# Kernel tuning notes

Measured on AMD Instinct MI355X. Metric: run time of the kernel, lower is better.

The kernel has to match this reference:

```python
import jax, jax.numpy as jnp
import numpy as np

N_NODES = 100000
N_EDGES = 1600000
IN_CH = 50


def setup_inputs() -> dict:
    key = jax.random.key(0)
    ks = jax.random.split(key, 6)
    x = jax.random.normal(ks[0], (N_NODES, IN_CH), dtype=jnp.float32)
    edge_index = jax.random.randint(ks[1], (2, N_EDGES), 0, N_NODES, dtype=jnp.int32)
    # Glorot-ish scaled weights
    W1 = jax.random.normal(ks[2], (2 * IN_CH, 64), dtype=jnp.float32) * (1.0 / np.sqrt(2 * IN_CH))
    b1 = jnp.zeros((64,), jnp.float32)
    W2 = jax.random.normal(ks[3], (2 * 64, 32), dtype=jnp.float32) * (1.0 / np.sqrt(2 * 64))
    b2 = jnp.zeros((32,), jnp.float32)
    W3 = jax.random.normal(ks[4], (32, 1), dtype=jnp.float32) * (1.0 / np.sqrt(32))
    b3 = jnp.zeros((1,), jnp.float32)
    return {"x": x, "edge_index": edge_index, "W1": W1, "b1": b1,
            "W2": W2, "b2": b2, "W3": W3, "b3": b3}


def _sage_conv(x, src, dst, W, b, n_nodes):
    # mean aggregation of neighbor (source) features onto target nodes
    msg = x[src]                                             # [E, d] gather
    agg = jax.ops.segment_sum(msg, dst, num_segments=n_nodes)  # [N, d]
    cnt = jax.ops.segment_sum(jnp.ones(src.shape[0], x.dtype), dst,
                              num_segments=n_nodes)            # [N]
    mean = agg / jnp.maximum(cnt, 1.0)[:, None]
    h = jnp.concatenate([x, mean], axis=-1)                  # concat=True
    return h @ W + b


def reference(x, edge_index, W1, b1, W2, b2, W3, b3):
    src, dst = edge_index[0], edge_index[1]
    n = x.shape[0]
    h = jax.nn.relu(_sage_conv(x, src, dst, W1, b1, n))
    h = jax.nn.relu(_sage_conv(h, src, dst, W2, b2, n))
    return h @ W3 + b3  # [N, 1]
```

## Files before the change

### kernel.cpp

```cpp
#include <hip/hip_runtime.h>
#include <hip/hip_bf16.h>

#define N_NODES 100000
#define N_EDGES 1600000
#define IN_CH 50
#define NPB 256
#define NB ((N_NODES + NPB - 1) / NPB)
#define CAPLOG 13
#define EPB 4096
#define NBLK_A ((N_EDGES + EPB - 1) / EPB)
#define PAD_BLOCKS ((N_NODES * 64) / 1024)

__global__ __launch_bounds__(1024) void bin_pad_kernel(
    const int* __restrict__ src, const int* __restrict__ dst,
    int* __restrict__ cursor_rel, unsigned* __restrict__ binned,
    const float* __restrict__ x, unsigned short* __restrict__ xb) {
    if (blockIdx.x >= NBLK_A) {
        int t = (blockIdx.x - NBLK_A) * 1024 + threadIdx.x;
        int n = t >> 6, c = t & 63;
        float v = (c < IN_CH) ? x[n * IN_CH + c] : 0.0f;
        __hip_bfloat16 hb = __float2bfloat16(v);
        xb[t] = *(unsigned short*)&hb;
        return;
    }
    __shared__ int bc[NB];
    __shared__ int boff[NB];
    int t = threadIdx.x;
    if (t < NB) bc[t] = 0;
    __syncthreads();
    int e0 = blockIdx.x * EPB;
    int e1 = min(e0 + EPB, N_EDGES);
    for (int i = e0 + t; i < e1; i += 1024)
        atomicAdd(&bc[dst[i] >> 8], 1);
    __syncthreads();
    if (t < NB) {
        int v = bc[t];
        int rel = v ? atomicAdd(&cursor_rel[t], v) : 0;
        boff[t] = (t << CAPLOG) + rel;
        bc[t] = 0;
    }
    __syncthreads();
    for (int i = e0 + t; i < e1; i += 1024) {
        int d = dst[i];
        int b = d >> 8;
        int k = atomicAdd(&bc[b], 1);
        binned[boff[b] + k] = ((unsigned)(d & 255) << 17) | (unsigned)src[i];
    }
}

__global__ __launch_bounds__(1024) void bucket_fine(
    const unsigned* __restrict__ binned, const int* __restrict__ cursor_rel,
    int* __restrict__ cnt, int* __restrict__ row_start, int* __restrict__ csr_src) {
    __shared__ int lcnt[NPB];
    __shared__ int lofs[NPB];
    __shared__ int sc[NPB];
    int t = threadIdx.x;
    int b = blockIdx.x;
    int nbase = b * NPB;
    int bbase = b << CAPLOG;
    int ecnt  = cursor_rel[b];
    if (t < NPB) lcnt[t] = 0;
    __syncthreads();
    for (int i = t; i < ecnt; i += 1024)
        atomicAdd(&lcnt[(binned[bbase + i] >> 17) & 255], 1);
    __syncthreads();
    int v = (t < NPB) ? lcnt[t] : 0;
    if (t < NPB) sc[t] = v;
    __syncthreads();
    for (int off = 1; off < NPB; off <<= 1) {
        int tmp = (t < NPB && t >= off) ? sc[t - off] : 0;
        __syncthreads();
        if (t < NPB) sc[t] += tmp;
        __syncthreads();
    }
    if (t < NPB) {
        int excl = sc[t] - v;
        lofs[t] = excl;
        int n = nbase + t;
        if (n < N_NODES) { cnt[n] = v; row_start[n] = bbase + excl; }
    }
    __syncthreads();
    for (int i = t; i < ecnt; i += 1024) {
        unsigned p = binned[bbase + i];
        int d = (int)((p >> 17) & 255);
        int k = atomicAdd(&lofs[d], 1);
        csr_src[bbase + k] = (int)(p & 0x1FFFFu);
    }
}

__device__ __forceinline__ void upadd8(float* a, uint4 v, float p) {
    a[0] = fmaf(p, __uint_as_float(v.x << 16), a[0]);
    a[1] = fmaf(p, __uint_as_float(v.x & 0xffff0000u), a[1]);
    a[2] = fmaf(p, __uint_as_float(v.y << 16), a[2]);
    a[3] = fmaf(p, __uint_as_float(v.y & 0xffff0000u), a[3]);
    a[4] = fmaf(p, __uint_as_float(v.z << 16), a[4]);
    a[5] = fmaf(p, __uint_as_float(v.z & 0xffff0000u), a[5]);
    a[6] = fmaf(p, __uint_as_float(v.w << 16), a[6]);
    a[7] = fmaf(p, __uint_as_float(v.w & 0xffff0000u), a[7]);
}

#define WAVE_LDS_FENCE() __asm__ volatile("s_waitcnt lgkmcnt(0)" ::: "memory")

__device__ __forceinline__ void gather2(
    const unsigned short* __restrict__ featb, const int* __restrict__ csr_src,
    const int* __restrict__ row_start, const int* __restrict__ cnt,
    int nb, int lane, float acc[2][8]) {
    int g  = lane >> 3;
    int cw = (lane & 7) * 8;
    int start[2], deg[2], sv[2];
    #pragma unroll
    for (int i = 0; i < 2; ++i) {
        start[i] = row_start[nb + i];
        deg[i]   = cnt[nb + i];
        #pragma unroll
        for (int c = 0; c < 8; ++c) acc[i][c] = 0.f;
    }
    int dmax = max(deg[0], deg[1]);
    #pragma unroll
    for (int i = 0; i < 2; ++i)
        sv[i] = (lane < deg[i]) ? csr_src[start[i] + lane] : 0;

    #pragma unroll
    for (int cb = 0; cb < 64; cb += 16) {
        if (cb >= dmax) break;
        int s00 = __shfl(sv[0], cb + g);
        int s01 = __shfl(sv[0], cb + 8 + g);
        int s10 = __shfl(sv[1], cb + g);
        int s11 = __shfl(sv[1], cb + 8 + g);
        uint4 v00 = *(const uint4*)(featb + s00 * 64 + cw);
        uint4 v01 = *(const uint4*)(featb + s01 * 64 + cw);
        uint4 v10 = *(const uint4*)(featb + s10 * 64 + cw);
        uint4 v11 = *(const uint4*)(featb + s11 * 64 + cw);
        int rem0 = deg[0] - cb;
        int rem1 = deg[1] - cb;
        upadd8(acc[0], v00, (g < rem0) ? 1.f : 0.f);
        upadd8(acc[0], v01, (g + 8 < rem0) ? 1.f : 0.f);
        upadd8(acc[1], v10, (g < rem1) ? 1.f : 0.f);
        upadd8(acc[1], v11, (g + 8 < rem1) ? 1.f : 0.f);
    }
    if (dmax > 64) {
        for (int i = 0; i < 2; ++i) {
            for (int c0 = 64; c0 < deg[i]; c0 += 64) {
                int rem = deg[i] - c0; if (rem > 64) rem = 64;
                int sx = (lane < rem) ? csr_src[start[i] + c0 + lane] : 0;
                for (int cb = 0; cb < rem; cb += 16) {
                    int s0 = __shfl(sx, cb + g);
                    int s1 = __shfl(sx, cb + 8 + g);
                    float p0 = (cb + g < rem) ? 1.f : 0.f;
                    float p1 = (cb + 8 + g < rem) ? 1.f : 0.f;
                    uint4 v0 = *(const uint4*)(featb + s0 * 64 + cw);
                    uint4 v1 = *(const uint4*)(featb + s1 * 64 + cw);
                    upadd8(acc[i], v0, p0);
                    upadd8(acc[i], v1, p1);
                }
            }
        }
    }
    #pragma unroll
    for (int i = 0; i < 2; ++i) {
        float inv = 1.0f / fmaxf((float)deg[i], 1.0f);
        #pragma unroll
        for (int c = 0; c < 8; ++c) {
            float t = acc[i][c];
            t += __shfl_xor(t, 8);
            t += __shfl_xor(t, 16);
            t += __shfl_xor(t, 32);
            acc[i][c] = t * inv;
        }
    }
}

__device__ __forceinline__ float bf16u(unsigned short u) {
    return __uint_as_float(((unsigned)u) << 16);
}

__global__ __launch_bounds__(256, 8) void layer1_fused(
    const unsigned short* __restrict__ xb,
    const int* __restrict__ csr_src, const int* __restrict__ row_start,
    const int* __restrict__ cnt, const float* __restrict__ W1,
    const float* __restrict__ b1, unsigned short* __restrict__ h1b) {
    int wv   = threadIdx.x >> 6;
    int lane = threadIdx.x & 63;
    int nb   = (blockIdx.x * 4 + wv) * 2;

    float acc[2][8];
    gather2(xb, csr_src, row_start, cnt, nb, lane, acc);

    __shared__ __align__(16) float selfF[4][2][64];
    __shared__ __align__(16) float meanF[4][2][64];
    #pragma unroll
    for (int i = 0; i < 2; ++i) {
        selfF[wv][i][lane] = bf16u(xb[((nb + i) << 6) + lane]);
        if (lane < 8) {
            *(float4*)&meanF[wv][i][lane * 8] =
                make_float4(acc[i][0], acc[i][1], acc[i][2], acc[i][3]);
            *(float4*)&meanF[wv][i][lane * 8 + 4] =
                make_float4(acc[i][4], acc[i][5], acc[i][6], acc[i][7]);
        }
    }
    WAVE_LDS_FENCE();

    float ao[2];
    float bb = b1[lane];
    #pragma unroll
    for (int i = 0; i < 2; ++i) ao[i] = bb;
    #pragma unroll
    for (int k = 0; k < IN_CH; ++k) {
        float w = W1[k * 64 + lane];
        #pragma unroll
        for (int i = 0; i < 2; ++i) ao[i] = fmaf(selfF[wv][i][k], w, ao[i]);
    }
    #pragma unroll
    for (int k = 0; k < IN_CH; ++k) {
        float w = W1[(IN_CH + k) * 64 + lane];
        #pragma unroll
        for (int i = 0; i < 2; ++i) ao[i] = fmaf(meanF[wv][i][k], w, ao[i]);
    }
    #pragma unroll
    for (int i = 0; i < 2; ++i) {
        float r = fmaxf(ao[i], 0.f);
        __hip_bfloat16 hb = __float2bfloat16(r);
        h1b[((nb + i) << 6) + lane] = *(unsigned short*)&hb;
    }
}

__global__ __launch_bounds__(256) void transform_w2(
    const unsigned short* __restrict__ h1b,
    const float* __restrict__ W2, const float* __restrict__ b2,
    unsigned short* __restrict__ y2b, float* __restrict__ yselff) {
    __shared__ __align__(16) float sW2[4096];
    int t = threadIdx.x;
    #pragma unroll
    for (int i = 0; i < 16; ++i)
        sW2[t + i * 256] = W2[t + i * 256];
    __syncthreads();

    int lane = t & 63;
    int wv   = t >> 6;
    int hh   = lane >> 5;
    int j    = lane & 31;
    int node = blockIdx.x * 8 + wv * 2 + hh;
    unsigned hp = *(const unsigned*)(h1b + node * 64 + j * 2);
    float ys = b2[j], ym = 0.f;
    #pragma unroll
    for (int kk = 0; kk < 32; ++kk) {
        unsigned hv = __shfl(hp, kk, 32);
        float h0 = __uint_as_float(hv << 16);
        float h1 = __uint_as_float(hv & 0xffff0000u);
        ys = fmaf(h0, sW2[(2 * kk) * 32 + j], ys);
        ym = fmaf(h0, sW2[(64 + 2 * kk) * 32 + j], ym);
        ys = fmaf(h1, sW2[(2 * kk + 1) * 32 + j], ys);
        ym = fmaf(h1, sW2[(64 + 2 * kk + 1) * 32 + j], ym);
    }
    yselff[node * 32 + j] = ys;
    __hip_bfloat16 hb = __float2bfloat16(ym);
    y2b[node * 32 + j] = *(unsigned short*)&hb;
}

__global__ __launch_bounds__(256, 8) void layer23_fused(
    const unsigned short* __restrict__ y2b,
    const int* __restrict__ csr_src, const int* __restrict__ row_start,
    const int* __restrict__ cnt, const float* __restrict__ yselff,
    const float* __restrict__ W3, const float* __restrict__ b3,
    float* __restrict__ out) {
    int wv   = threadIdx.x >> 6;
    int lane = threadIdx.x & 63;
    int nb   = (blockIdx.x * 4 + wv) * 2;
    int g  = lane >> 2;
    int cw = (lane & 3) * 8;

    int start[2], deg[2], sv[2];
    float acc[2][8];
    #pragma unroll
    for (int i = 0; i < 2; ++i) {
        start[i] = row_start[nb + i];
        deg[i]   = cnt[nb + i];
        #pragma unroll
        for (int c = 0; c < 8; ++c) acc[i][c] = 0.f;
    }
    int dmax = max(deg[0], deg[1]);
    #pragma unroll
    for (int i = 0; i < 2; ++i)
        sv[i] = (lane < deg[i]) ? csr_src[start[i] + lane] : 0;

    #pragma unroll
    for (int cb = 0; cb < 64; cb += 32) {
        if (cb >= dmax) break;
        int s00 = __shfl(sv[0], cb + g);
        int s01 = __shfl(sv[0], cb + 16 + g);
        int s10 = __shfl(sv[1], cb + g);
        int s11 = __shfl(sv[1], cb + 16 + g);
        uint4 v00 = *(const uint4*)(y2b + s00 * 32 + cw);
        uint4 v01 = *(const uint4*)(y2b + s01 * 32 + cw);
        uint4 v10 = *(const uint4*)(y2b + s10 * 32 + cw);
        uint4 v11 = *(const uint4*)(y2b + s11 * 32 + cw);
        int rem0 = deg[0] - cb;
        int rem1 = deg[1] - cb;
        upadd8(acc[0], v00, (g < rem0) ? 1.f : 0.f);
        upadd8(acc[0], v01, (g + 16 < rem0) ? 1.f : 0.f);
        upadd8(acc[1], v10, (g < rem1) ? 1.f : 0.f);
        upadd8(acc[1], v11, (g + 16 < rem1) ? 1.f : 0.f);
    }
    if (dmax > 64) {
        for (int i = 0; i < 2; ++i) {
            for (int c0 = 64; c0 < deg[i]; c0 += 64) {
                int rem = deg[i] - c0; if (rem > 64) rem = 64;
                int sx = (lane < rem) ? csr_src[start[i] + c0 + lane] : 0;
                for (int cb = 0; cb < rem; cb += 32) {
                    int s0 = __shfl(sx, cb + g);
                    int s1 = __shfl(sx, cb + 16 + g);
                    float p0 = (cb + g < rem) ? 1.f : 0.f;
                    float p1 = (cb + 16 + g < rem) ? 1.f : 0.f;
                    uint4 v0 = *(const uint4*)(y2b + s0 * 32 + cw);
                    uint4 v1 = *(const uint4*)(y2b + s1 * 32 + cw);
                    upadd8(acc[i], v0, p0);
                    upadd8(acc[i], v1, p1);
                }
            }
        }
    }

    __shared__ __align__(16) float aggF[4][2][32];
    #pragma unroll
    for (int i = 0; i < 2; ++i) {
        float inv = 1.0f / fmaxf((float)deg[i], 1.0f);
        #pragma unroll
        for (int c = 0; c < 8; ++c) {
            float t = acc[i][c];
            t += __shfl_xor(t, 4);
            t += __shfl_xor(t, 8);
            t += __shfl_xor(t, 16);
            t += __shfl_xor(t, 32);
            acc[i][c] = t * inv;
        }
    }
    if (lane < 4) {
        #pragma unroll
        for (int i = 0; i < 2; ++i) {
            *(float4*)&aggF[wv][i][lane * 8] =
                make_float4(acc[i][0], acc[i][1], acc[i][2], acc[i][3]);
            *(float4*)&aggF[wv][i][lane * 8 + 4] =
                make_float4(acc[i][4], acc[i][5], acc[i][6], acc[i][7]);
        }
    }
    WAVE_LDS_FENCE();

    int hh = lane >> 5;
    int j  = lane & 31;
    float pre = yselff[(nb + hh) * 32 + j] + aggF[wv][hh][j];
    float v0 = fmaxf(pre, 0.f) * W3[j];
    #pragma unroll
    for (int off = 1; off <= 16; off <<= 1)
        v0 += __shfl_xor(v0, off);
    if (j == 0)
        out[nb + hh] = v0 + b3[0];
}

extern "C" void kernel_launch(void* const* d_in, const int* in_sizes, int n_in,
                              void* d_out, int out_size, void* d_ws, size_t ws_size,
                              hipStream_t stream) {
    const float* x   = (const float*)d_in[0];
    const int*   ei  = (const int*)d_in[1];
    const int*   src = ei;
    const int*   dst = ei + N_EDGES;
    const float* W1  = (const float*)d_in[2];
    const float* b1  = (const float*)d_in[3];
    const float* W2  = (const float*)d_in[4];
    const float* b2  = (const float*)d_in[5];
    const float* W3  = (const float*)d_in[6];
    const float* b3  = (const float*)d_in[7];
    float* out = (float*)d_out;

    char* ws = (char*)d_ws;
    auto align = [](size_t v) { return (v + 255) & ~(size_t)255; };
    size_t o = 0;
    int* cursor_rel = (int*)(ws + o); o = align(o + 512 * 4);
    int* cnt       = (int*)(ws + o); o = align(o + (size_t)N_NODES * 4);
    int* row_start = (int*)(ws + o); o = align(o + (size_t)N_NODES * 4);
    unsigned* binned = (unsigned*)(ws + o); o = align(o + ((size_t)NB << CAPLOG) * 4);
    int* csr_src   = (int*)(ws + o); o = align(o + ((size_t)NB << CAPLOG) * 4);
    unsigned short* xb  = (unsigned short*)(ws + o); o = align(o + (size_t)N_NODES * 64 * 2);
    unsigned short* h1b = (unsigned short*)(ws + o); o = align(o + (size_t)N_NODES * 64 * 2);
    unsigned short* y2b = (unsigned short*)(ws + o); o = align(o + (size_t)N_NODES * 32 * 2);
    float* yselff = (float*)(ws + o); o = align(o + (size_t)N_NODES * 32 * 4);

    (void)hipMemsetAsync(cursor_rel, 0, 512 * sizeof(int), stream);

    bin_pad_kernel<<<NBLK_A + PAD_BLOCKS, 1024, 0, stream>>>(src, dst, cursor_rel,
                                                             binned, x, xb);
    bucket_fine<<<NB, 1024, 0, stream>>>(binned, cursor_rel, cnt, row_start, csr_src);

    layer1_fused<<<N_NODES / 8, 256, 0, stream>>>(xb, csr_src, row_start, cnt,
                                                  W1, b1, h1b);
    transform_w2<<<N_NODES / 8, 256, 0, stream>>>(h1b, W2, b2, y2b, yselff);
    layer23_fused<<<N_NODES / 8, 256, 0, stream>>>(y2b, csr_src, row_start, cnt,
                                                   yselff, W3, b3, out);
}
```

Before: 264.7 us.

## Replace bucketed CSR build with global-atomic count/scan/scatter; restructure W2 transform

```diff
diff --git a/kernel.cpp b/kernel.cpp
--- a/kernel.cpp
+++ b/kernel.cpp
@@ -4,16 +4,12 @@
 #define N_NODES 100000
 #define N_EDGES 1600000
 #define IN_CH 50
-#define NPB 256
-#define NB ((N_NODES + NPB - 1) / NPB)
-#define CAPLOG 13
 #define EPB 4096
 #define NBLK_A ((N_EDGES + EPB - 1) / EPB)
 #define PAD_BLOCKS ((N_NODES * 64) / 1024)
 
-__global__ __launch_bounds__(1024) void bin_pad_kernel(
-    const int* __restrict__ src, const int* __restrict__ dst,
-    int* __restrict__ cursor_rel, unsigned* __restrict__ binned,
+__global__ __launch_bounds__(1024) void count_pad(
+    const int* __restrict__ dst, int* __restrict__ cnt,
     const float* __restrict__ x, unsigned short* __restrict__ xb) {
     if (blockIdx.x >= NBLK_A) {
         int t = (blockIdx.x - NBLK_A) * 1024 + threadIdx.x;
@@ -23,68 +19,41 @@
         xb[t] = *(unsigned short*)&hb;
         return;
     }
-    __shared__ int bc[NB];
-    __shared__ int boff[NB];
-    int t = threadIdx.x;
-    if (t < NB) bc[t] = 0;
-    __syncthreads();
     int e0 = blockIdx.x * EPB;
     int e1 = min(e0 + EPB, N_EDGES);
-    for (int i = e0 + t; i < e1; i += 1024)
-        atomicAdd(&bc[dst[i] >> 8], 1);
-    __syncthreads();
-    if (t < NB) {
-        int v = bc[t];
-        int rel = v ? atomicAdd(&cursor_rel[t], v) : 0;
-        boff[t] = (t << CAPLOG) + rel;
-        bc[t] = 0;
-    }
-    __syncthreads();
-    for (int i = e0 + t; i < e1; i += 1024) {
+    for (int i = e0 + threadIdx.x; i < e1; i += 1024)
+        atomicAdd(&cnt[dst[i]], 1);
+}
+
+__global__ __launch_bounds__(256) void alloc_rows(
+    const int* __restrict__ cnt, int* __restrict__ row_start,
+    int* __restrict__ gcur) {
+    int n = blockIdx.x * 256 + threadIdx.x;
+    int lane = threadIdx.x & 63;
+    int v = (n < N_NODES) ? cnt[n] : 0;
+    int s = v;
+    #pragma unroll
+    for (int off = 1; off < 64; off <<= 1) {
+        int t = __shfl_up(s, off);
+        if (lane >= off) s += t;
+    }
+    int total = __shfl(s, 63);
+    int base = 0;
+    if (lane == 63) base = atomicAdd(gcur, total);
+    base = __shfl(base, 63);
+    if (n < N_NODES) row_start[n] = base + s - v;
+}
+
+__global__ __launch_bounds__(1024) void scatter_csr(
+    const int* __restrict__ src, const int* __restrict__ dst,
+    const int* __restrict__ row_start, int* __restrict__ cur,
+    int* __restrict__ csr_src) {
+    int e0 = blockIdx.x * EPB;
+    int e1 = min(e0 + EPB, N_EDGES);
+    for (int i = e0 + threadIdx.x; i < e1; i += 1024) {
         int d = dst[i];
-        int b = d >> 8;
-        int k = atomicAdd(&bc[b], 1);
-        binned[boff[b] + k] = ((unsigned)(d & 255) << 17) | (unsigned)src[i];
-    }
-}
-
-__global__ __launch_bounds__(1024) void bucket_fine(
-    const unsigned* __restrict__ binned, const int* __restrict__ cursor_rel,
-    int* __restrict__ cnt, int* __restrict__ row_start, int* __restrict__ csr_src) {
-    __shared__ int lcnt[NPB];
-    __shared__ int lofs[NPB];
-    __shared__ int sc[NPB];
-    int t = threadIdx.x;
-    int b = blockIdx.x;
-    int nbase = b * NPB;
-    int bbase = b << CAPLOG;
-    int ecnt  = cursor_rel[b];
-    if (t < NPB) lcnt[t] = 0;
-    __syncthreads();
-    for (int i = t; i < ecnt; i += 1024)
-        atomicAdd(&lcnt[(binned[bbase + i] >> 17) & 255], 1);
-    __syncthreads();
-    int v = (t < NPB) ? lcnt[t] : 0;
-    if (t < NPB) sc[t] = v;
-    __syncthreads();
-    for (int off = 1; off < NPB; off <<= 1) {
-        int tmp = (t < NPB && t >= off) ? sc[t - off] : 0;
-        __syncthreads();
-        if (t < NPB) sc[t] += tmp;
-        __syncthreads();
-    }
-    if (t < NPB) {
-        int excl = sc[t] - v;
-        lofs[t] = excl;
-        int n = nbase + t;
-        if (n < N_NODES) { cnt[n] = v; row_start[n] = bbase + excl; }
-    }
-    __syncthreads();
-    for (int i = t; i < ecnt; i += 1024) {
-        unsigned p = binned[bbase + i];
-        int d = (int)((p >> 17) & 255);
-        int k = atomicAdd(&lofs[d], 1);
-        csr_src[bbase + k] = (int)(p & 0x1FFFFu);
+        int k = atomicAdd(&cur[d], 1);
+        csr_src[row_start[d] + k] = src[i];
     }
 }
 
@@ -228,33 +197,47 @@
     const unsigned short* __restrict__ h1b,
     const float* __restrict__ W2, const float* __restrict__ b2,
     unsigned short* __restrict__ y2b, float* __restrict__ yselff) {
-    __shared__ __align__(16) float sW2[4096];
-    int t = threadIdx.x;
-    #pragma unroll
-    for (int i = 0; i < 16; ++i)
-        sW2[t + i * 256] = W2[t + i * 256];
-    __syncthreads();
-
+    __shared__ __align__(16) float hrowF[4][4][64];
+    int t    = threadIdx.x;
+    int wv   = t >> 6;
     int lane = t & 63;
-    int wv   = t >> 6;
-    int hh   = lane >> 5;
-    int j    = lane & 31;
-    int node = blockIdx.x * 8 + wv * 2 + hh;
-    unsigned hp = *(const unsigned*)(h1b + node * 64 + j * 2);
-    float ys = b2[j], ym = 0.f;
-    #pragma unroll
-    for (int kk = 0; kk < 32; ++kk) {
-        unsigned hv = __shfl(hp, kk, 32);
-        float h0 = __uint_as_float(hv << 16);
-        float h1 = __uint_as_float(hv & 0xffff0000u);
-        ys = fmaf(h0, sW2[(2 * kk) * 32 + j], ys);
-        ym = fmaf(h0, sW2[(64 + 2 * kk) * 32 + j], ym);
-        ys = fmaf(h1, sW2[(2 * kk + 1) * 32 + j], ys);
-        ym = fmaf(h1, sW2[(64 + 2 * kk + 1) * 32 + j], ym);
-    }
-    yselff[node * 32 + j] = ys;
-    __hip_bfloat16 hb = __float2bfloat16(ym);
-    y2b[node * 32 + j] = *(unsigned short*)&hb;
+    int nb4  = blockIdx.x * 16 + wv * 4;
+
+    {
+        int in = lane >> 4, q = lane & 15;
+        uint2 hv = *(const uint2*)(h1b + (nb4 + in) * 64 + q * 4);
+        float4 f;
+        f.x = __uint_as_float(hv.x << 16);
+        f.y = __uint_as_float(hv.x & 0xffff0000u);
+        f.z = __uint_as_float(hv.y << 16);
+        f.w = __uint_as_float(hv.y & 0xffff0000u);
+        *(float4*)&hrowF[wv][in][q * 4] = f;
+    }
+    WAVE_LDS_FENCE();
+
+    int jj  = lane & 31;
+    int sel = lane >> 5;
+    const float* Wp = W2 + sel * 64 * 32 + jj;
+    float a[4] = {0.f, 0.f, 0.f, 0.f};
+    #pragma unroll
+    for (int k = 0; k < 64; ++k) {
+        float w = Wp[k * 32];
+        #pragma unroll
+        for (int i = 0; i < 4; ++i)
+            a[i] = fmaf(hrowF[wv][i][k], w, a[i]);
+    }
+    if (sel == 0) {
+        float bb = b2[jj];
+        #pragma unroll
+        for (int i = 0; i < 4; ++i)
+            yselff[(nb4 + i) * 32 + jj] = a[i] + bb;
+    } else {
+        #pragma unroll
+        for (int i = 0; i < 4; ++i) {
+            __hip_bfloat16 hb = __float2bfloat16(a[i]);
+            y2b[(nb4 + i) * 32 + jj] = *(unsigned short*)&hb;
+        }
+    }
 }
 
 __global__ __launch_bounds__(256, 8) void layer23_fused(
@@ -374,25 +357,27 @@
     char* ws = (char*)d_ws;
     auto align = [](size_t v) { return (v + 255) & ~(size_t)255; };
     size_t o = 0;
-    int* cursor_rel = (int*)(ws + o); o = align(o + 512 * 4);
+    int* gcur      = (int*)(ws + o); o = align(o + 512 * 4);
     int* cnt       = (int*)(ws + o); o = align(o + (size_t)N_NODES * 4);
     int* row_start = (int*)(ws + o); o = align(o + (size_t)N_NODES * 4);
-    unsigned* binned = (unsigned*)(ws + o); o = align(o + ((size_t)NB << CAPLOG) * 4);
-    int* csr_src   = (int*)(ws + o); o = align(o + ((size_t)NB << CAPLOG) * 4);
+    int* cur       = (int*)(ws + o); o = align(o + (size_t)N_NODES * 4);
+    int* csr_src   = (int*)(ws + o); o = align(o + (size_t)N_EDGES * 4);
     unsigned short* xb  = (unsigned short*)(ws + o); o = align(o + (size_t)N_NODES * 64 * 2);
     unsigned short* h1b = (unsigned short*)(ws + o); o = align(o + (size_t)N_NODES * 64 * 2);
     unsigned short* y2b = (unsigned short*)(ws + o); o = align(o + (size_t)N_NODES * 32 * 2);
     float* yselff = (float*)(ws + o); o = align(o + (size_t)N_NODES * 32 * 4);
 
-    (void)hipMemsetAsync(cursor_rel, 0, 512 * sizeof(int), stream);
-
-    bin_pad_kernel<<<NBLK_A + PAD_BLOCKS, 1024, 0, stream>>>(src, dst, cursor_rel,
-                                                             binned, x, xb);
-    bucket_fine<<<NB, 1024, 0, stream>>>(binned, cursor_rel, cnt, row_start, csr_src);
+    (void)hipMemsetAsync(gcur, 0, 512 * sizeof(int), stream);
+    (void)hipMemsetAsync(cnt, 0, (size_t)N_NODES * sizeof(int), stream);
+    (void)hipMemsetAsync(cur, 0, (size_t)N_NODES * sizeof(int), stream);
+
+    count_pad<<<NBLK_A + PAD_BLOCKS, 1024, 0, stream>>>(dst, cnt, x, xb);
+    alloc_rows<<<(N_NODES + 255) / 256, 256, 0, stream>>>(cnt, row_start, gcur);
+    scatter_csr<<<NBLK_A, 1024, 0, stream>>>(src, dst, row_start, cur, csr_src);
 
     layer1_fused<<<N_NODES / 8, 256, 0, stream>>>(xb, csr_src, row_start, cnt,
                                                   W1, b1, h1b);
-    transform_w2<<<N_NODES / 8, 256, 0, stream>>>(h1b, W2, b2, y2b, yselff);
+    transform_w2<<<N_NODES / 16, 256, 0, stream>>>(h1b, W2, b2, y2b, yselff);
     layer23_fused<<<N_NODES / 8, 256, 0, stream>>>(y2b, csr_src, row_start, cnt,
                                                    yselff, W3, b3, out);
 }
```

New measurement: 375.2 us. 1.42x slower.
